# Performance work log

Measured on AMD Instinct MI355X. Metric: run time of the kernel, lower is better.

## Reference

```python
import jax, jax.numpy as jnp
import numpy as np

N = 100000
E = 640000
D = 128
L = 3
B = 128
OUT = 10


def setup_inputs() -> dict:
    key = jax.random.key(0)
    ks = jax.random.split(key, 8)
    x = jax.random.normal(ks[0], (N, D), dtype=jnp.float32)
    edge_index = jax.random.randint(ks[1], (2, E), 0, N, dtype=jnp.int64)
    batch = jnp.sort(jax.random.randint(ks[2], (N,), 0, B, dtype=jnp.int64))
    # per-layer GCNConv weights (in==hidden==D so they stack) and biases
    Ws = jax.random.normal(ks[3], (L, D, D), dtype=jnp.float32) / np.sqrt(D)
    bs = jnp.zeros((L, D), dtype=jnp.float32)
    # MLP head: single Linear(hidden -> out), norm=None
    W_mlp = jax.random.normal(ks[4], (D, OUT), dtype=jnp.float32) / np.sqrt(D)
    b_mlp = jnp.zeros((OUT,), dtype=jnp.float32)
    return {"x": x, "edge_index": edge_index, "batch": batch,
            "Ws": Ws, "bs": bs, "W_mlp": W_mlp, "b_mlp": b_mlp}


def reference(x, edge_index, batch, Ws, bs, W_mlp, b_mlp):
    n = x.shape[0]
    # --- GCN normalization (PyG gcn_norm with self-loops, edge_weight=1) ---
    loop = jnp.arange(n, dtype=edge_index.dtype)
    src = jnp.concatenate([edge_index[0], loop])  # message sources (x_j)
    dst = jnp.concatenate([edge_index[1], loop])  # aggregation targets
    deg = jax.ops.segment_sum(jnp.ones_like(dst, dtype=x.dtype), dst, num_segments=n)
    dinv = jnp.where(deg > 0, jax.lax.rsqrt(jnp.maximum(deg, 1.0)), 0.0)
    norm = dinv[src] * dinv[dst]  # [E+N]

    def gcn_conv(h, W, b):
        hw = h @ W  # [N, D] dense transform
        msg = hw[src] * norm[:, None]  # gather + scale [E+N, D]
        agg = jax.ops.segment_sum(msg, dst, num_segments=n)  # scatter-add
        return agg + b

    h = x
    for l in range(Ws.shape[0]):
        h = jax.nn.relu(gcn_conv(h, Ws[l], bs[l]))

    # global add pool over graphs
    pooled = jax.ops.segment_sum(h, batch, num_segments=B)  # [B, D]
    # MLP head (single linear, no norm/act)
    return pooled @ W_mlp + b_mlp
```

## Files before the change

### kernel.cpp

```cpp
#include <hip/hip_runtime.h>
#include <hip/hip_bf16.h>

#define N_NODES 100000
#define N_EDGES 640000
#define DIM 128
#define N_LAYERS 3
#define N_GRAPHS 128
#define N_OUT 10
#define SCAN_BLK 1024
#define N_SCAN_BLKS ((N_NODES + SCAN_BLK - 1) / SCAN_BLK)
#define PCHUNK 128

typedef _Float16 h4 __attribute__((ext_vector_type(4)));
typedef _Float16 h2 __attribute__((ext_vector_type(2)));
typedef _Float16 h8 __attribute__((ext_vector_type(8)));
typedef float f32x4 __attribute__((ext_vector_type(4)));

struct EdgeRec { int s; float w; };


__global__ void hist_dst(const int* __restrict__ ei, int* __restrict__ cnt) {
    int e = blockIdx.x * blockDim.x + threadIdx.x;
    if (e < N_EDGES) atomicAdd(&cnt[ei[N_EDGES + e]], 1);
}

__global__ void make_dinv(const int* __restrict__ cnt, float* __restrict__ dinv) {
    int i = blockIdx.x * blockDim.x + threadIdx.x;
    if (i < N_NODES) dinv[i] = rsqrtf((float)(cnt[i] + 1));
}


__global__ void scan1(const int* __restrict__ cnt, int* __restrict__ off, int* __restrict__ bsum) {
    __shared__ int tmp[256];
    int base = blockIdx.x * SCAN_BLK + threadIdx.x * 4;
    int c[4];
    #pragma unroll
    for (int k = 0; k < 4; ++k) c[k] = (base + k < N_NODES) ? cnt[base + k] : 0;
    int tot = c[0] + c[1] + c[2] + c[3];
    tmp[threadIdx.x] = tot;
    __syncthreads();
    int val = tot;
    for (int d = 1; d < 256; d <<= 1) {
        int add = (threadIdx.x >= d) ? tmp[threadIdx.x - d] : 0;
        __syncthreads();
        val += add;
        tmp[threadIdx.x] = val;
        __syncthreads();
    }
    int ex = val - tot;
    int e1 = ex + c[0], e2 = e1 + c[1], e3 = e2 + c[2];
    if (base + 0 < N_NODES) off[base + 0] = ex;
    if (base + 1 < N_NODES) off[base + 1] = e1;
    if (base + 2 < N_NODES) off[base + 2] = e2;
    if (base + 3 < N_NODES) off[base + 3] = e3;
    if (threadIdx.x == 255) bsum[blockIdx.x] = val;
}

__global__ void scan2(int* __restrict__ bsum) {
    if (threadIdx.x == 0 && blockIdx.x == 0) {
        int acc = 0;
        for (int i = 0; i < N_SCAN_BLKS; ++i) { int v = bsum[i]; bsum[i] = acc; acc += v; }
    }
}

__global__ void scan3(int* __restrict__ off, const int* __restrict__ bsum) {
    int i = blockIdx.x * blockDim.x + threadIdx.x;
    if (i < N_NODES) off[i] += bsum[i / SCAN_BLK];
    if (i == 0) off[N_NODES] = N_EDGES;
}


__global__ void fill_csr(const int* __restrict__ ei, const float* __restrict__ dinv,
                         const int* __restrict__ off, int* __restrict__ cursor,
                         EdgeRec* __restrict__ csr) {
    int e = blockIdx.x * blockDim.x + threadIdx.x;
    if (e >= N_EDGES) return;
    int s = ei[e], d = ei[N_EDGES + e];
    int pos = off[d] + atomicAdd(&cursor[d], 1);
    EdgeRec r; r.s = s; r.w = dinv[s] * dinv[d];
    csr[pos] = r;
}


__global__ void wt_prep(const float* __restrict__ Ws, _Float16* __restrict__ wt) {
    int t = blockIdx.x * blockDim.x + threadIdx.x;
    if (t >= N_LAYERS * DIM * 32) return;
    int u = t & 31;
    int n = (t >> 5) & 127;
    int l = t >> 12;
    const float* W = Ws + (size_t)l * DIM * DIM;
    int k0 = u * 4;
    h4 v;
    v.x = (_Float16)W[(k0 + 0) * DIM + n];
    v.y = (_Float16)W[(k0 + 1) * DIM + n];
    v.z = (_Float16)W[(k0 + 2) * DIM + n];
    v.w = (_Float16)W[(k0 + 3) * DIM + n];
    int du = u ^ (n & 31);
    ((h4*)wt)[(size_t)l * 4096 + n * 32 + du] = v;
}


__device__ __forceinline__ h4 loadfrag(const _Float16* p) { return *(const h4*)p; }
__device__ __forceinline__ h4 loadfrag(const float* p) {
    float4 f = *(const float4*)p;
    h4 v; v.x = (_Float16)f.x; v.y = (_Float16)f.y; v.z = (_Float16)f.z; v.w = (_Float16)f.w;
    return v;
}

template<typename TIN>
__global__ __launch_bounds__(256) void gemm_mfma(const TIN* __restrict__ in,
                                                 const _Float16* __restrict__ wt,
                                                 _Float16* __restrict__ out) {
    __shared__ h4 Wl[4096];
    {
        const float4* src = (const float4*)wt;
        float4* dst = (float4*)Wl;
        #pragma unroll
        for (int i = 0; i < 8; ++i) dst[threadIdx.x + i * 256] = src[threadIdx.x + i * 256];
    }
    __syncthreads();

    const int wave = threadIdx.x >> 6;
    const int lane = threadIdx.x & 63;
    const int m0 = blockIdx.x * 64 + wave * 16;
    if (m0 >= N_NODES) return;

    const int row = lane & 15;
    const int g   = lane >> 4;
    const int m   = m0 + row;
    const TIN* arow = in + (size_t)m * DIM;

    f32x4 acc[8] = {};

    #pragma unroll
    for (int kc = 0; kc < 8; ++kc) {
        const int k = kc * 16 + g * 4;
        const h4 bfrag = loadfrag(arow + k);
        const int u = kc * 4 + g;
        #pragma unroll
        for (int nb = 0; nb < 8; ++nb) {
            const int n = nb * 16 + row;
            const h4 afrag = Wl[n * 32 + (u ^ (n & 31))];
            acc[nb] = __builtin_amdgcn_mfma_f32_16x16x16f16(afrag, bfrag, acc[nb], 0, 0, 0);
        }
    }

    _Float16* orow = out + (size_t)m * DIM;
    #pragma unroll
    for (int nb = 0; nb < 8; ++nb) {
        h4 v;
        v.x = (_Float16)acc[nb].x; v.y = (_Float16)acc[nb].y;
        v.z = (_Float16)acc[nb].z; v.w = (_Float16)acc[nb].w;
        ((h4*)orow)[nb * 4 + g] = v;
    }
}


__global__ __launch_bounds__(256) void gather_agg(const _Float16* __restrict__ hw,
                                                  const float* __restrict__ dinv,
                                                  const int* __restrict__ off,
                                                  const EdgeRec* __restrict__ csr,
                                                  const float* __restrict__ bias,
                                                  _Float16* __restrict__ hout) {
    const int i = (blockIdx.x * blockDim.x + threadIdx.x) >> 6;
    if (i >= N_NODES) return;
    const int lane = threadIdx.x & 63;
    const int q   = lane >> 4;
    const int sub = lane & 15;
    const h8* hw8 = (const h8*)hw;

    const int beg = off[i], end = off[i + 1];
    float accf[8] = {0.f, 0.f, 0.f, 0.f, 0.f, 0.f, 0.f, 0.f};

    if (q == 3) {
        float di = dinv[i];
        float w = di * di;
        h8 v = hw8[(size_t)i * 16 + sub];
        #pragma unroll
        for (int d = 0; d < 8; ++d) accf[d] = w * (float)v[d];
    }

    int j = beg + q;
    for (; j + 4 < end; j += 8) {
        EdgeRec e0 = csr[j];
        EdgeRec e1 = csr[j + 4];
        h8 v0 = hw8[(size_t)e0.s * 16 + sub];
        h8 v1 = hw8[(size_t)e1.s * 16 + sub];
        #pragma unroll
        for (int d = 0; d < 8; ++d) accf[d] += e0.w * (float)v0[d] + e1.w * (float)v1[d];
    }
    for (; j < end; j += 4) {
        EdgeRec e0 = csr[j];
        h8 v0 = hw8[(size_t)e0.s * 16 + sub];
        #pragma unroll
        for (int d = 0; d < 8; ++d) accf[d] += e0.w * (float)v0[d];
    }

    #pragma unroll
    for (int d = 0; d < 8; ++d) {
        float a = accf[d];
        a += __shfl_xor(a, 16);
        a += __shfl_xor(a, 32);
        accf[d] = a;
    }

    if (q == 0) {
        const float4 b0 = *(const float4*)&bias[sub * 8];
        const float4 b1 = *(const float4*)&bias[sub * 8 + 4];
        h8 v;
        v[0] = (_Float16)fmaxf(accf[0] + b0.x, 0.0f);
        v[1] = (_Float16)fmaxf(accf[1] + b0.y, 0.0f);
        v[2] = (_Float16)fmaxf(accf[2] + b0.z, 0.0f);
        v[3] = (_Float16)fmaxf(accf[3] + b0.w, 0.0f);
        v[4] = (_Float16)fmaxf(accf[4] + b1.x, 0.0f);
        v[5] = (_Float16)fmaxf(accf[5] + b1.y, 0.0f);
        v[6] = (_Float16)fmaxf(accf[6] + b1.z, 0.0f);
        v[7] = (_Float16)fmaxf(accf[7] + b1.w, 0.0f);
        ((h8*)hout)[(size_t)i * 16 + sub] = v;
    }
}


__global__ __launch_bounds__(256) void pool_chunk(const _Float16* __restrict__ h,
                                                  const int* __restrict__ batch,
                                                  float* __restrict__ pooled) {
    const int base = blockIdx.x * PCHUNK;
    const int t = threadIdx.x;
    const int lane4 = t & 31;
    const int rgrp = t >> 5;
    const h4* hp = (const h4*)h;

    float a0 = 0.f, a1 = 0.f, a2 = 0.f, a3 = 0.f;
    int cur = -1;
    const int rend = (base + PCHUNK < N_NODES) ? base + PCHUNK : N_NODES;
    for (int r = base + rgrp; r < rend; r += 8) {
        int b = batch[r];
        if (b != cur) {
            if (cur >= 0) {
                float* pp = &pooled[cur * DIM + lane4 * 4];
                atomicAdd(pp + 0, a0); atomicAdd(pp + 1, a1);
                atomicAdd(pp + 2, a2); atomicAdd(pp + 3, a3);
            }
            cur = b; a0 = a1 = a2 = a3 = 0.f;
        }
        h4 v = hp[(size_t)r * 32 + lane4];
        a0 += (float)v.x; a1 += (float)v.y; a2 += (float)v.z; a3 += (float)v.w;
    }
    if (cur >= 0) {
        float* pp = &pooled[cur * DIM + lane4 * 4];
        atomicAdd(pp + 0, a0); atomicAdd(pp + 1, a1);
        atomicAdd(pp + 2, a2); atomicAdd(pp + 3, a3);
    }
}


__global__ void mlp_head(const float* __restrict__ pooled, const float* __restrict__ Wm,
                         const float* __restrict__ bm, float* __restrict__ out) {
    int t = blockIdx.x * blockDim.x + threadIdx.x;
    if (t >= N_GRAPHS * N_OUT) return;
    int b = t / N_OUT;
    int o = t % N_OUT;
    float acc = bm[o];
    #pragma unroll 8
    for (int k = 0; k < DIM; ++k) acc += pooled[b * DIM + k] * Wm[k * N_OUT + o];
    out[t] = acc;
}


extern "C" void kernel_launch(void* const* d_in, const int* in_sizes, int n_in,
                              void* d_out, int out_size, void* d_ws, size_t ws_size,
                              hipStream_t stream) {
    const float* x     = (const float*)d_in[0];
    const int*   ei    = (const int*)d_in[1];
    const int*   batch = (const int*)d_in[2];
    const float* Ws    = (const float*)d_in[3];
    const float* bs    = (const float*)d_in[4];
    const float* Wm    = (const float*)d_in[5];
    const float* bm    = (const float*)d_in[6];
    float* out = (float*)d_out;

    char* p = (char*)d_ws;
    int*      cnt     = (int*)p;        p += N_NODES * 4;
    int*      cursor  = (int*)p;        p += N_NODES * 4;
    float*    dinv    = (float*)p;      p += N_NODES * 4;
    int*      csr_off = (int*)p;        p += (N_NODES + 16) * 4;
    int*      bsum    = (int*)p;        p += 128 * 4;
    _Float16* wt      = (_Float16*)p;   p += (size_t)N_LAYERS * DIM * DIM * 2;
    EdgeRec*  csr     = (EdgeRec*)p;    p += (size_t)N_EDGES * 8;
    _Float16* bufA    = (_Float16*)p;   p += (size_t)N_NODES * DIM * 2;
    _Float16* bufB    = (_Float16*)p;   p += (size_t)N_NODES * DIM * 2;
    float*    pooled  = (float*)p;      p += N_GRAPHS * DIM * 4;

    const int nnode_blk = (N_NODES + 255) / 256;
    const int nedge_blk = (N_EDGES + 255) / 256;

    hipMemsetAsync(cnt, 0, N_NODES * 8, stream);
    hipMemsetAsync(pooled, 0, N_GRAPHS * DIM * 4, stream);

    hist_dst<<<nedge_blk, 256, 0, stream>>>(ei, cnt);
    make_dinv<<<nnode_blk, 256, 0, stream>>>(cnt, dinv);
    wt_prep<<<(N_LAYERS * DIM * 32 + 255) / 256, 256, 0, stream>>>(Ws, wt);

    scan1<<<N_SCAN_BLKS, 256, 0, stream>>>(cnt, csr_off, bsum);
    scan2<<<1, 64, 0, stream>>>(bsum);
    scan3<<<nnode_blk, 256, 0, stream>>>(csr_off, bsum);

    fill_csr<<<nedge_blk, 256, 0, stream>>>(ei, dinv, csr_off, cursor, csr);

    const int gemm_grid = (N_NODES + 63) / 64;
    const int gather_grid = (N_NODES * 64 + 255) / 256;
    for (int l = 0; l < N_LAYERS; ++l) {
        if (l == 0) gemm_mfma<float><<<gemm_grid, 256, 0, stream>>>(x, wt, bufA);
        else        gemm_mfma<_Float16><<<gemm_grid, 256, 0, stream>>>(bufB, wt + (size_t)l * DIM * DIM, bufA);
        gather_agg<<<gather_grid, 256, 0, stream>>>(bufA, dinv, csr_off, csr, bs + l * DIM, bufB);
    }

    pool_chunk<<<(N_NODES + PCHUNK - 1) / PCHUNK, 256, 0, stream>>>(bufB, batch, pooled);
    mlp_head<<<(N_GRAPHS * N_OUT + 255) / 256, 256, 0, stream>>>(pooled, Wm, bm, out);
}
```

Baseline: 299.6 us.

## Use packed fp16 gather accumulation and two row tiles per GEMM wave

The CSR edge weight is now stored as a duplicated fp16 pair, and gather_agg accumulates with packed half2 multiply-adds instead of converting each element to fp32. The lane mapping is reorganised into four edge streams, each covering two 8-lane halves of the row, and streams are reduced with shuffles over 8 and 16. The GEMM now computes 32 rows per wave, so each LDS weight fragment feeds two MFMAs, and the grid is halved. Accumulating aggregations in fp16 cuts ALU and conversion work but loses precision and raises overflow risk. The larger GEMM tile also raises register pressure.

```diff
diff --git a/kernel.cpp b/kernel.cpp
--- a/kernel.cpp
+++ b/kernel.cpp
@@ -16,7 +16,7 @@
 typedef _Float16 h8 __attribute__((ext_vector_type(8)));
 typedef float f32x4 __attribute__((ext_vector_type(4)));
 
-struct EdgeRec { int s; float w; };
+struct EdgeRec { int s; unsigned int w2; };
 
 
 __global__ void hist_dst(const int* __restrict__ ei, int* __restrict__ cnt) {
@@ -77,7 +77,9 @@
     if (e >= N_EDGES) return;
     int s = ei[e], d = ei[N_EDGES + e];
     int pos = off[d] + atomicAdd(&cursor[d], 1);
-    EdgeRec r; r.s = s; r.w = dinv[s] * dinv[d];
+    float w = dinv[s] * dinv[d];
+    h2 w2; w2.x = (_Float16)w; w2.y = (_Float16)w;
+    EdgeRec r; r.s = s; r.w2 = *(unsigned int*)&w2;
     csr[pos] = r;
 }
 
@@ -122,39 +124,55 @@
 
     const int wave = threadIdx.x >> 6;
     const int lane = threadIdx.x & 63;
-    const int m0 = blockIdx.x * 64 + wave * 16;
+    const int m0 = blockIdx.x * 128 + wave * 32;
     if (m0 >= N_NODES) return;
 
     const int row = lane & 15;
     const int g   = lane >> 4;
-    const int m   = m0 + row;
-    const TIN* arow = in + (size_t)m * DIM;
-
-    f32x4 acc[8] = {};
+    const TIN* arow0 = in + (size_t)(m0 + row) * DIM;
+    const TIN* arow1 = arow0 + (size_t)16 * DIM;
+
+    f32x4 acc0[8] = {};
+    f32x4 acc1[8] = {};
 
     #pragma unroll
     for (int kc = 0; kc < 8; ++kc) {
         const int k = kc * 16 + g * 4;
-        const h4 bfrag = loadfrag(arow + k);
+        const h4 b0 = loadfrag(arow0 + k);
+        const h4 b1 = loadfrag(arow1 + k);
         const int u = kc * 4 + g;
         #pragma unroll
         for (int nb = 0; nb < 8; ++nb) {
             const int n = nb * 16 + row;
             const h4 afrag = Wl[n * 32 + (u ^ (n & 31))];
-            acc[nb] = __builtin_amdgcn_mfma_f32_16x16x16f16(afrag, bfrag, acc[nb], 0, 0, 0);
+            acc0[nb] = __builtin_amdgcn_mfma_f32_16x16x16f16(afrag, b0, acc0[nb], 0, 0, 0);
+            acc1[nb] = __builtin_amdgcn_mfma_f32_16x16x16f16(afrag, b1, acc1[nb], 0, 0, 0);
         }
     }
 
-    _Float16* orow = out + (size_t)m * DIM;
+    _Float16* orow0 = out + (size_t)(m0 + row) * DIM;
+    _Float16* orow1 = orow0 + (size_t)16 * DIM;
     #pragma unroll
     for (int nb = 0; nb < 8; ++nb) {
-        h4 v;
-        v.x = (_Float16)acc[nb].x; v.y = (_Float16)acc[nb].y;
-        v.z = (_Float16)acc[nb].z; v.w = (_Float16)acc[nb].w;
-        ((h4*)orow)[nb * 4 + g] = v;
-    }
-}
-
+        h4 v0, v1;
+        v0.x = (_Float16)acc0[nb].x; v0.y = (_Float16)acc0[nb].y;
+        v0.z = (_Float16)acc0[nb].z; v0.w = (_Float16)acc0[nb].w;
+        v1.x = (_Float16)acc1[nb].x; v1.y = (_Float16)acc1[nb].y;
+        v1.z = (_Float16)acc1[nb].z; v1.w = (_Float16)acc1[nb].w;
+        ((h4*)orow0)[nb * 4 + g] = v0;
+        ((h4*)orow1)[nb * 4 + g] = v1;
+    }
+}
+
+
+__device__ __forceinline__ h8 fma_pairs(h8 v, unsigned int w2bits, h8 a) {
+    h2 w2 = *(h2*)&w2bits;
+    h2* vp = (h2*)&v;
+    h2* ap = (h2*)&a;
+    #pragma unroll
+    for (int p = 0; p < 4; ++p) ap[p] += vp[p] * w2;
+    return a;
+}
 
 __global__ __launch_bounds__(256) void gather_agg(const _Float16* __restrict__ hw,
                                                   const float* __restrict__ dinv,
@@ -165,58 +183,59 @@
     const int i = (blockIdx.x * blockDim.x + threadIdx.x) >> 6;
     if (i >= N_NODES) return;
     const int lane = threadIdx.x & 63;
-    const int q   = lane >> 4;
-    const int sub = lane & 15;
+    const int grp    = lane >> 3;
+    const int stream = grp & 3;
+    const int half   = grp >> 2;
+    const int sub    = lane & 7;
+    const int idx8   = half * 8 + sub;
     const h8* hw8 = (const h8*)hw;
 
     const int beg = off[i], end = off[i + 1];
-    float accf[8] = {0.f, 0.f, 0.f, 0.f, 0.f, 0.f, 0.f, 0.f};
-
-    if (q == 3) {
+    h8 acc = {};
+
+    if (stream == 3) {
         float di = dinv[i];
         float w = di * di;
-        h8 v = hw8[(size_t)i * 16 + sub];
-        #pragma unroll
-        for (int d = 0; d < 8; ++d) accf[d] = w * (float)v[d];
-    }
-
-    int j = beg + q;
+        h2 w2; w2.x = (_Float16)w; w2.y = (_Float16)w;
+        acc = fma_pairs(hw8[(size_t)i * 16 + idx8], *(unsigned int*)&w2, acc);
+    }
+
+    int j = beg + stream;
     for (; j + 4 < end; j += 8) {
         EdgeRec e0 = csr[j];
         EdgeRec e1 = csr[j + 4];
-        h8 v0 = hw8[(size_t)e0.s * 16 + sub];
-        h8 v1 = hw8[(size_t)e1.s * 16 + sub];
-        #pragma unroll
-        for (int d = 0; d < 8; ++d) accf[d] += e0.w * (float)v0[d] + e1.w * (float)v1[d];
+        h8 v0 = hw8[(size_t)e0.s * 16 + idx8];
+        h8 v1 = hw8[(size_t)e1.s * 16 + idx8];
+        acc = fma_pairs(v0, e0.w2, acc);
+        acc = fma_pairs(v1, e1.w2, acc);
     }
     for (; j < end; j += 4) {
         EdgeRec e0 = csr[j];
-        h8 v0 = hw8[(size_t)e0.s * 16 + sub];
-        #pragma unroll
-        for (int d = 0; d < 8; ++d) accf[d] += e0.w * (float)v0[d];
-    }
-
+        acc = fma_pairs(hw8[(size_t)e0.s * 16 + idx8], e0.w2, acc);
+    }
+
+    float a[8];
     #pragma unroll
     for (int d = 0; d < 8; ++d) {
-        float a = accf[d];
-        a += __shfl_xor(a, 16);
-        a += __shfl_xor(a, 32);
-        accf[d] = a;
-    }
-
-    if (q == 0) {
-        const float4 b0 = *(const float4*)&bias[sub * 8];
-        const float4 b1 = *(const float4*)&bias[sub * 8 + 4];
+        float v = (float)acc[d];
+        v += __shfl_xor(v, 8);
+        v += __shfl_xor(v, 16);
+        a[d] = v;
+    }
+
+    if (stream == 0) {
+        const float4 b0 = *(const float4*)&bias[half * 64 + sub * 8];
+        const float4 b1 = *(const float4*)&bias[half * 64 + sub * 8 + 4];
         h8 v;
-        v[0] = (_Float16)fmaxf(accf[0] + b0.x, 0.0f);
-        v[1] = (_Float16)fmaxf(accf[1] + b0.y, 0.0f);
-        v[2] = (_Float16)fmaxf(accf[2] + b0.z, 0.0f);
-        v[3] = (_Float16)fmaxf(accf[3] + b0.w, 0.0f);
-        v[4] = (_Float16)fmaxf(accf[4] + b1.x, 0.0f);
-        v[5] = (_Float16)fmaxf(accf[5] + b1.y, 0.0f);
-        v[6] = (_Float16)fmaxf(accf[6] + b1.z, 0.0f);
-        v[7] = (_Float16)fmaxf(accf[7] + b1.w, 0.0f);
-        ((h8*)hout)[(size_t)i * 16 + sub] = v;
+        v[0] = (_Float16)fmaxf(a[0] + b0.x, 0.0f);
+        v[1] = (_Float16)fmaxf(a[1] + b0.y, 0.0f);
+        v[2] = (_Float16)fmaxf(a[2] + b0.z, 0.0f);
+        v[3] = (_Float16)fmaxf(a[3] + b0.w, 0.0f);
+        v[4] = (_Float16)fmaxf(a[4] + b1.x, 0.0f);
+        v[5] = (_Float16)fmaxf(a[5] + b1.y, 0.0f);
+        v[6] = (_Float16)fmaxf(a[6] + b1.z, 0.0f);
+        v[7] = (_Float16)fmaxf(a[7] + b1.w, 0.0f);
+        ((h8*)hout)[(size_t)i * 16 + idx8] = v;
     }
 }
 
@@ -307,7 +326,7 @@
 
     fill_csr<<<nedge_blk, 256, 0, stream>>>(ei, dinv, csr_off, cursor, csr);
 
-    const int gemm_grid = (N_NODES + 63) / 64;
+    const int gemm_grid = (N_NODES + 127) / 128;
     const int gather_grid = (N_NODES * 64 + 255) / 256;
     for (int l = 0; l < N_LAYERS; ++l) {
         if (l == 0) gemm_mfma<float><<<gemm_grid, 256, 0, stream>>>(x, wt, bufA);
```

Result: slower. 308.8 us (+3.1%).

## Factor GCN edge norm into per-node scaling and accumulate gathers in fp16

Applied to the files above, without the earlier changes.

The symmetric normalization dinv[s]*dinv[d] is split in two: the GEMM epilogue scales each row by dinv[src], and the aggregation scales the sum by dinv[dst]. The CSR therefore stores only source indices, which halves edge-record traffic. Aggregation now adds packed fp16 pairs, with lanes regrouped into four edge streams of two 64-dim halves, and reduces across streams with shuffles. The change also fuses make_dinv into scan1 and parallelizes scan2. Summing in fp16 risks precision loss and overflow on high-degree nodes.

```diff
diff --git a/kernel.cpp b/kernel.cpp
--- a/kernel.cpp
+++ b/kernel.cpp
@@ -16,26 +16,23 @@
 typedef _Float16 h8 __attribute__((ext_vector_type(8)));
 typedef float f32x4 __attribute__((ext_vector_type(4)));
 
-struct EdgeRec { int s; float w; };
-
 
 __global__ void hist_dst(const int* __restrict__ ei, int* __restrict__ cnt) {
     int e = blockIdx.x * blockDim.x + threadIdx.x;
     if (e < N_EDGES) atomicAdd(&cnt[ei[N_EDGES + e]], 1);
 }
 
-__global__ void make_dinv(const int* __restrict__ cnt, float* __restrict__ dinv) {
-    int i = blockIdx.x * blockDim.x + threadIdx.x;
-    if (i < N_NODES) dinv[i] = rsqrtf((float)(cnt[i] + 1));
-}
-
-
-__global__ void scan1(const int* __restrict__ cnt, int* __restrict__ off, int* __restrict__ bsum) {
+
+__global__ void scan1(const int* __restrict__ cnt, int* __restrict__ off, int* __restrict__ bsum,
+                      float* __restrict__ dinv) {
     __shared__ int tmp[256];
     int base = blockIdx.x * SCAN_BLK + threadIdx.x * 4;
     int c[4];
     #pragma unroll
     for (int k = 0; k < 4; ++k) c[k] = (base + k < N_NODES) ? cnt[base + k] : 0;
+    #pragma unroll
+    for (int k = 0; k < 4; ++k)
+        if (base + k < N_NODES) dinv[base + k] = rsqrtf((float)(c[k] + 1));
     int tot = c[0] + c[1] + c[2] + c[3];
     tmp[threadIdx.x] = tot;
     __syncthreads();
@@ -57,10 +54,20 @@
 }
 
 __global__ void scan2(int* __restrict__ bsum) {
-    if (threadIdx.x == 0 && blockIdx.x == 0) {
-        int acc = 0;
-        for (int i = 0; i < N_SCAN_BLKS; ++i) { int v = bsum[i]; bsum[i] = acc; acc += v; }
-    }
+    __shared__ int tmp[128];
+    int t = threadIdx.x;
+    int v = (t < N_SCAN_BLKS) ? bsum[t] : 0;
+    int own = v;
+    tmp[t] = v;
+    __syncthreads();
+    for (int d = 1; d < 128; d <<= 1) {
+        int add = (t >= d) ? tmp[t - d] : 0;
+        __syncthreads();
+        v += add;
+        tmp[t] = v;
+        __syncthreads();
+    }
+    if (t < N_SCAN_BLKS) bsum[t] = v - own;
 }
 
 __global__ void scan3(int* __restrict__ off, const int* __restrict__ bsum) {
@@ -70,15 +77,13 @@
 }
 
 
-__global__ void fill_csr(const int* __restrict__ ei, const float* __restrict__ dinv,
-                         const int* __restrict__ off, int* __restrict__ cursor,
-                         EdgeRec* __restrict__ csr) {
+__global__ void fill_csr(const int* __restrict__ ei, const int* __restrict__ off,
+                         int* __restrict__ cursor, int* __restrict__ csr_src) {
     int e = blockIdx.x * blockDim.x + threadIdx.x;
     if (e >= N_EDGES) return;
     int s = ei[e], d = ei[N_EDGES + e];
     int pos = off[d] + atomicAdd(&cursor[d], 1);
-    EdgeRec r; r.s = s; r.w = dinv[s] * dinv[d];
-    csr[pos] = r;
+    csr_src[pos] = s;
 }
 
 
@@ -110,6 +115,7 @@
 template<typename TIN>
 __global__ __launch_bounds__(256) void gemm_mfma(const TIN* __restrict__ in,
                                                  const _Float16* __restrict__ wt,
+                                                 const float* __restrict__ dinv,
                                                  _Float16* __restrict__ out) {
     __shared__ h4 Wl[4096];
     {
@@ -129,6 +135,7 @@
     const int g   = lane >> 4;
     const int m   = m0 + row;
     const TIN* arow = in + (size_t)m * DIM;
+    const float di = dinv[m];
 
     f32x4 acc[8] = {};
 
@@ -149,8 +156,8 @@
     #pragma unroll
     for (int nb = 0; nb < 8; ++nb) {
         h4 v;
-        v.x = (_Float16)acc[nb].x; v.y = (_Float16)acc[nb].y;
-        v.z = (_Float16)acc[nb].z; v.w = (_Float16)acc[nb].w;
+        v.x = (_Float16)(acc[nb].x * di); v.y = (_Float16)(acc[nb].y * di);
+        v.z = (_Float16)(acc[nb].z * di); v.w = (_Float16)(acc[nb].w * di);
         ((h4*)orow)[nb * 4 + g] = v;
     }
 }
@@ -159,64 +166,66 @@
 __global__ __launch_bounds__(256) void gather_agg(const _Float16* __restrict__ hw,
                                                   const float* __restrict__ dinv,
                                                   const int* __restrict__ off,
-                                                  const EdgeRec* __restrict__ csr,
+                                                  const int* __restrict__ csr_src,
                                                   const float* __restrict__ bias,
                                                   _Float16* __restrict__ hout) {
     const int i = (blockIdx.x * blockDim.x + threadIdx.x) >> 6;
     if (i >= N_NODES) return;
     const int lane = threadIdx.x & 63;
-    const int q   = lane >> 4;
-    const int sub = lane & 15;
+    const int grp    = lane >> 3;
+    const int stream = grp & 3;
+    const int half   = grp >> 2;
+    const int sub    = lane & 7;
+    const int idx8   = half * 8 + sub;
     const h8* hw8 = (const h8*)hw;
 
     const int beg = off[i], end = off[i + 1];
-    float accf[8] = {0.f, 0.f, 0.f, 0.f, 0.f, 0.f, 0.f, 0.f};
-
-    if (q == 3) {
-        float di = dinv[i];
-        float w = di * di;
-        h8 v = hw8[(size_t)i * 16 + sub];
+    h8 acc = {};
+
+    if (stream == 3) acc = hw8[(size_t)i * 16 + idx8];
+
+    int j = beg + stream;
+    for (; j + 4 < end; j += 8) {
+        int s0 = csr_src[j];
+        int s1 = csr_src[j + 4];
+        h8 v0 = hw8[(size_t)s0 * 16 + idx8];
+        h8 v1 = hw8[(size_t)s1 * 16 + idx8];
         #pragma unroll
-        for (int d = 0; d < 8; ++d) accf[d] = w * (float)v[d];
-    }
-
-    int j = beg + q;
-    for (; j + 4 < end; j += 8) {
-        EdgeRec e0 = csr[j];
-        EdgeRec e1 = csr[j + 4];
-        h8 v0 = hw8[(size_t)e0.s * 16 + sub];
-        h8 v1 = hw8[(size_t)e1.s * 16 + sub];
+        for (int p = 0; p < 4; ++p) {
+            ((h2*)&acc)[p] += ((h2*)&v0)[p];
+            ((h2*)&acc)[p] += ((h2*)&v1)[p];
+        }
+    }
+    for (; j < end; j += 4) {
+        int s0 = csr_src[j];
+        h8 v0 = hw8[(size_t)s0 * 16 + idx8];
         #pragma unroll
-        for (int d = 0; d < 8; ++d) accf[d] += e0.w * (float)v0[d] + e1.w * (float)v1[d];
-    }
-    for (; j < end; j += 4) {
-        EdgeRec e0 = csr[j];
-        h8 v0 = hw8[(size_t)e0.s * 16 + sub];
-        #pragma unroll
-        for (int d = 0; d < 8; ++d) accf[d] += e0.w * (float)v0[d];
-    }
-
-    #pragma unroll
-    for (int d = 0; d < 8; ++d) {
-        float a = accf[d];
-        a += __shfl_xor(a, 16);
-        a += __shfl_xor(a, 32);
-        accf[d] = a;
-    }
-
-    if (q == 0) {
-        const float4 b0 = *(const float4*)&bias[sub * 8];
-        const float4 b1 = *(const float4*)&bias[sub * 8 + 4];
+        for (int p = 0; p < 4; ++p) ((h2*)&acc)[p] += ((h2*)&v0)[p];
+    }
+
+    unsigned int* au = (unsigned int*)&acc;
+    #pragma unroll
+    for (int p = 0; p < 4; ++p) {
+        unsigned int o = __shfl_xor(au[p], 8);
+        h2 a = *(h2*)&au[p]; a += *(h2*)&o; au[p] = *(unsigned int*)&a;
+        o = __shfl_xor(au[p], 16);
+        h2 b = *(h2*)&au[p]; b += *(h2*)&o; au[p] = *(unsigned int*)&b;
+    }
+
+    if (stream == 0) {
+        const float di = dinv[i];
+        const float4 b0 = *(const float4*)&bias[half * 64 + sub * 8];
+        const float4 b1 = *(const float4*)&bias[half * 64 + sub * 8 + 4];
         h8 v;
-        v[0] = (_Float16)fmaxf(accf[0] + b0.x, 0.0f);
-        v[1] = (_Float16)fmaxf(accf[1] + b0.y, 0.0f);
-        v[2] = (_Float16)fmaxf(accf[2] + b0.z, 0.0f);
-        v[3] = (_Float16)fmaxf(accf[3] + b0.w, 0.0f);
-        v[4] = (_Float16)fmaxf(accf[4] + b1.x, 0.0f);
-        v[5] = (_Float16)fmaxf(accf[5] + b1.y, 0.0f);
-        v[6] = (_Float16)fmaxf(accf[6] + b1.z, 0.0f);
-        v[7] = (_Float16)fmaxf(accf[7] + b1.w, 0.0f);
-        ((h8*)hout)[(size_t)i * 16 + sub] = v;
+        v[0] = (_Float16)fmaxf((float)acc[0] * di + b0.x, 0.0f);
+        v[1] = (_Float16)fmaxf((float)acc[1] * di + b0.y, 0.0f);
+        v[2] = (_Float16)fmaxf((float)acc[2] * di + b0.z, 0.0f);
+        v[3] = (_Float16)fmaxf((float)acc[3] * di + b0.w, 0.0f);
+        v[4] = (_Float16)fmaxf((float)acc[4] * di + b1.x, 0.0f);
+        v[5] = (_Float16)fmaxf((float)acc[5] * di + b1.y, 0.0f);
+        v[6] = (_Float16)fmaxf((float)acc[6] * di + b1.z, 0.0f);
+        v[7] = (_Float16)fmaxf((float)acc[7] * di + b1.w, 0.0f);
+        ((h8*)hout)[(size_t)i * 16 + idx8] = v;
     }
 }
 
@@ -286,7 +295,7 @@
     int*      csr_off = (int*)p;        p += (N_NODES + 16) * 4;
     int*      bsum    = (int*)p;        p += 128 * 4;
     _Float16* wt      = (_Float16*)p;   p += (size_t)N_LAYERS * DIM * DIM * 2;
-    EdgeRec*  csr     = (EdgeRec*)p;    p += (size_t)N_EDGES * 8;
+    int*      csr_src = (int*)p;        p += (size_t)N_EDGES * 4;
     _Float16* bufA    = (_Float16*)p;   p += (size_t)N_NODES * DIM * 2;
     _Float16* bufB    = (_Float16*)p;   p += (size_t)N_NODES * DIM * 2;
     float*    pooled  = (float*)p;      p += N_GRAPHS * DIM * 4;
@@ -298,21 +307,20 @@
     hipMemsetAsync(pooled, 0, N_GRAPHS * DIM * 4, stream);
 
     hist_dst<<<nedge_blk, 256, 0, stream>>>(ei, cnt);
-    make_dinv<<<nnode_blk, 256, 0, stream>>>(cnt, dinv);
     wt_prep<<<(N_LAYERS * DIM * 32 + 255) / 256, 256, 0, stream>>>(Ws, wt);
 
-    scan1<<<N_SCAN_BLKS, 256, 0, stream>>>(cnt, csr_off, bsum);
-    scan2<<<1, 64, 0, stream>>>(bsum);
+    scan1<<<N_SCAN_BLKS, 256, 0, stream>>>(cnt, csr_off, bsum, dinv);
+    scan2<<<1, 128, 0, stream>>>(bsum);
     scan3<<<nnode_blk, 256, 0, stream>>>(csr_off, bsum);
 
-    fill_csr<<<nedge_blk, 256, 0, stream>>>(ei, dinv, csr_off, cursor, csr);
+    fill_csr<<<nedge_blk, 256, 0, stream>>>(ei, csr_off, cursor, csr_src);
 
     const int gemm_grid = (N_NODES + 63) / 64;
     const int gather_grid = (N_NODES * 64 + 255) / 256;
     for (int l = 0; l < N_LAYERS; ++l) {
-        if (l == 0) gemm_mfma<float><<<gemm_grid, 256, 0, stream>>>(x, wt, bufA);
-        else        gemm_mfma<_Float16><<<gemm_grid, 256, 0, stream>>>(bufB, wt + (size_t)l * DIM * DIM, bufA);
-        gather_agg<<<gather_grid, 256, 0, stream>>>(bufA, dinv, csr_off, csr, bs + l * DIM, bufB);
+        if (l == 0) gemm_mfma<float><<<gemm_grid, 256, 0, stream>>>(x, wt, dinv, bufA);
+        else        gemm_mfma<_Float16><<<gemm_grid, 256, 0, stream>>>(bufB, wt + (size_t)l * DIM * DIM, dinv, bufA);
+        gather_agg<<<gather_grid, 256, 0, stream>>>(bufA, dinv, csr_off, csr_src, bs + l * DIM, bufB);
     }
 
     pool_chunk<<<(N_NODES + PCHUNK - 1) / PCHUNK, 256, 0, stream>>>(bufB, batch, pooled);
```

Result: no change. 301.4 us (+0.6%).
